# Kernel optimization log

Hardware: AMD Instinct MI355X
Metric: run time of the kernel (lower is better)

Reference implementation:

```python
import jax, jax.numpy as jnp
import numpy as np
import math

EMBED_DIM = 768
NUM_HEADS = 12
HEAD_DIM = EMBED_DIM // NUM_HEADS
SPARSITY = 0.1


def setup_inputs() -> dict:
    key = jax.random.key(0)
    ks = jax.random.split(key, 5)
    B, N, D = 4, 1024, EMBED_DIM
    s = 1.0 / math.sqrt(D)
    return {
        "x": jax.random.normal(ks[0], (B, N, D), dtype=jnp.float32),
        "W_qkv": jax.random.normal(ks[1], (D, 3 * D), dtype=jnp.float32) * s,
        "b_qkv": jnp.zeros((3 * D,), dtype=jnp.float32),
        "W_out": jax.random.normal(ks[2], (D, D), dtype=jnp.float32) * s,
        "b_out": jnp.zeros((D,), dtype=jnp.float32),
    }


def reference(x, W_qkv, b_qkv, W_out, b_out):
    B, N, D = x.shape
    H, hd = NUM_HEADS, HEAD_DIM
    qkv = x @ W_qkv + b_qkv                      # [B,N,3D]
    qkv = qkv.reshape(B, N, 3, H, hd).transpose(2, 0, 3, 1, 4)  # [3,B,H,N,hd]
    q, k, v = qkv[0], qkv[1], qkv[2]
    attn = jnp.einsum("bhqd,bhkd->bhqk", q, k) * (1.0 / math.sqrt(hd))  # [B,H,N,N]
    kth = int(N * N * SPARSITY)
    if kth > 0:
        # kth smallest value over the flattened per-(b,h) attention matrix
        flat = attn.reshape(B, H, N * N)
        thr = jnp.sort(flat, axis=-1)[..., kth - 1]               # [B,H]
        attn = jnp.where(attn <= thr[:, :, None, None], -1e9, attn)
    attn = jax.nn.softmax(attn, axis=-1)
    out = jnp.einsum("bhqk,bhkd->bhqd", attn, v)                  # [B,H,N,hd]
    out = out.transpose(0, 2, 1, 3).reshape(B, N, D)
    return out @ W_out + b_out
```

## Files before the change

kernel.cpp:

```cpp
#include <hip/hip_runtime.h>
#include <math.h>

#define SEQ 1024
#define DMODEL 768
#define NHEADS 12
#define HDIM 64
#define D3 2304
#define BH 48
#define NTOK 4096
#define KTH 104857u
#define NBIN 4096
#define BIN0 14336

typedef __bf16 bf16x8 __attribute__((ext_vector_type(8)));
typedef float  f32x4  __attribute__((ext_vector_type(4)));

#define SWZ(row, chunk) ((row) * 32 + (((chunk) ^ (((row) >> 1) & 3)) * 8))

__device__ __forceinline__ void gl16(const ushort* g, ushort* l) {
    __builtin_amdgcn_global_load_lds(
        (__attribute__((address_space(1))) void*)(size_t)(g),
        (__attribute__((address_space(3))) void*)(l), 16, 0, 0);
}

__device__ __forceinline__ void split1(float x, ushort& h, ushort& l) {
    unsigned b  = __float_as_uint(x);
    unsigned hb = (b + 0x7FFFu + ((b >> 16) & 1u)) >> 16;
    float hf = __uint_as_float(hb << 16);
    float r  = x - hf;
    unsigned rb = __float_as_uint(r);
    unsigned lb = (rb + 0x7FFFu + ((rb >> 16) & 1u)) >> 16;
    h = (ushort)hb; l = (ushort)lb;
}

__device__ __forceinline__ ushort bf16rne(float x) {
    unsigned b = __float_as_uint(x);
    return (ushort)((b + 0x7FFFu + ((b >> 16) & 1u)) >> 16);
}

__global__ __launch_bounds__(256) void k_xsplit(const float* __restrict__ x,
                                                ushort* __restrict__ xh,
                                                ushort* __restrict__ xl, int n,
                                                unsigned* __restrict__ hist) {
    int g = blockIdx.x * 256 + threadIdx.x;
    if (g < BH * NBIN) hist[g] = 0u;
    int i = g * 4;
    if (i >= n) return;
    float4 v = *(const float4*)(x + i);
    ushort4 h, l;
    split1(v.x, h.x, l.x); split1(v.y, h.y, l.y);
    split1(v.z, h.z, l.z); split1(v.w, h.w, l.w);
    *(ushort4*)(xh + i) = h;
    *(ushort4*)(xl + i) = l;
}

__global__ __launch_bounds__(256) void k_wsplit(const float* __restrict__ W,
                                                ushort* __restrict__ Wth,
                                                ushort* __restrict__ Wtl,
                                                int K, int N) {
    __shared__ float t[64][65];
    int k0 = blockIdx.y * 64, n0 = blockIdx.x * 64;
    int tid = threadIdx.x;
    int r = tid >> 4, c = (tid & 15) * 4;
#pragma unroll
    for (int u = 0; u < 4; u++) {
        int rr = r + u * 16;
        float4 v = *(const float4*)(W + (size_t)(k0 + rr) * N + n0 + c);
        t[rr][c] = v.x; t[rr][c + 1] = v.y; t[rr][c + 2] = v.z; t[rr][c + 3] = v.w;
    }
    __syncthreads();
    int n = tid >> 2, kc = (tid & 3) * 16;
    ushort hb[16] __attribute__((aligned(16)));
    ushort lb[16] __attribute__((aligned(16)));
#pragma unroll
    for (int j = 0; j < 16; j++) split1(t[kc + j][n], hb[j], lb[j]);
    ushort* dh = Wth + (size_t)(n0 + n) * K + k0 + kc;
    ushort* dl = Wtl + (size_t)(n0 + n) * K + k0 + kc;
    *(uint4*)(dh)     = *(uint4*)&hb[0];
    *(uint4*)(dh + 8) = *(uint4*)&hb[8];
    *(uint4*)(dl)     = *(uint4*)&lb[0];
    *(uint4*)(dl + 8) = *(uint4*)&lb[8];
}

#define STAGE_LDS(ko)                                                           \
    gl16(gAh + (ko), &sA[0][wbase]);                                            \
    gl16(gAh2 + (ko), &sA[0][2048 + wbase]);                                    \
    gl16(gAl + (ko), &sA[1][wbase]);                                            \
    gl16(gAl2 + (ko), &sA[1][2048 + wbase]);                                    \
    gl16(gBh + (ko), &sB[0][wbase]);                                            \
    gl16(gBh2 + (ko), &sB[0][2048 + wbase]);                                    \
    gl16(gBl + (ko), &sB[1][wbase]);                                            \
    gl16(gBl2 + (ko), &sB[1][2048 + wbase]);

#define GEMM_CORE_SETUP(Kdim)                                                   \
    __shared__ ushort sA[2][128 * 32];                                          \
    __shared__ ushort sB[2][128 * 32];                                          \
    int tid = threadIdx.x, lane = tid & 63, wave = tid >> 6;                    \
    int wm = (wave >> 1) * 64, wn = (wave & 1) * 64;                            \
    int l15 = lane & 15, q = lane >> 4;                                         \
    int sr = tid >> 2, sc = tid & 3;                                            \
    const int K = (Kdim);                                                       \
    int scs = sc ^ ((sr >> 1) & 3);          \
    const ushort* gAh = Ah + (size_t)(m0 + sr) * K + scs * 8;                   \
    const ushort* gAl = Al + (size_t)(m0 + sr) * K + scs * 8;                   \
    const ushort* gBh = Bh + (size_t)(n0 + sr) * K + scs * 8;                   \
    const ushort* gBl = Bl + (size_t)(n0 + sr) * K + scs * 8;                   \
    const ushort* gAh2 = gAh + (size_t)64 * K;                                  \
    const ushort* gAl2 = gAl + (size_t)64 * K;                                  \
    const ushort* gBh2 = gBh + (size_t)64 * K;                                  \
    const ushort* gBl2 = gBl + (size_t)64 * K;                                  \
    int wbase = wave * 512;              \
    f32x4 acc[4][4] = {};                                                       \
    STAGE_LDS(0)                                                                \
    __syncthreads();                                                            \
    const int NIT = K / 32;                                                     \
    for (int it = 0; it < NIT; ++it) {                                          \
        bf16x8 fah[4], fal[4], fbh[4], fbl[4];                                  \
        _Pragma("unroll")                                                       \
        for (int mt = 0; mt < 4; mt++) {                                        \
            int rr = wm + mt * 16 + l15;                                        \
            fah[mt] = *(const bf16x8*)(&sA[0][SWZ(rr, q)]);                     \
            fal[mt] = *(const bf16x8*)(&sA[1][SWZ(rr, q)]);                     \
        }                                                                       \
        _Pragma("unroll")                                                       \
        for (int nt = 0; nt < 4; nt++) {                                        \
            int rr = wn + nt * 16 + l15;                                        \
            fbh[nt] = *(const bf16x8*)(&sB[0][SWZ(rr, q)]);                     \
            fbl[nt] = *(const bf16x8*)(&sB[1][SWZ(rr, q)]);                     \
        }                                                                       \
        __syncthreads();                 \
        if (it + 1 < NIT) { STAGE_LDS((it + 1) * 32) }                          \
        _Pragma("unroll")                                                       \
        for (int mt = 0; mt < 4; mt++)                                          \
            _Pragma("unroll")                                                   \
            for (int nt = 0; nt < 4; nt++) {                                    \
                acc[mt][nt] = __builtin_amdgcn_mfma_f32_16x16x32_bf16(          \
                    fah[mt], fbh[nt], acc[mt][nt], 0, 0, 0);                    \
                acc[mt][nt] = __builtin_amdgcn_mfma_f32_16x16x32_bf16(          \
                    fah[mt], fbl[nt], acc[mt][nt], 0, 0, 0);                    \
                acc[mt][nt] = __builtin_amdgcn_mfma_f32_16x16x32_bf16(          \
                    fal[mt], fbh[nt], acc[mt][nt], 0, 0, 0);                    \
            }                                                                   \
        __syncthreads();                   \
    }

__global__ __launch_bounds__(256) void k_gemm_out(
    const ushort* __restrict__ Ah, const ushort* __restrict__ Al,
    const ushort* __restrict__ Bh, const ushort* __restrict__ Bl,
    const float* __restrict__ bias, float* __restrict__ C,
    int M, int N, int Kin) {
    int m0 = blockIdx.y * 128, n0 = blockIdx.x * 128;
    GEMM_CORE_SETUP(Kin)
#pragma unroll
    for (int nt = 0; nt < 4; nt++) {
        int col = n0 + wn + nt * 16 + l15;
        float bv = bias[col];
#pragma unroll
        for (int mt = 0; mt < 4; mt++) {
            int rowb = m0 + wm + mt * 16 + q * 4;
#pragma unroll
            for (int r = 0; r < 4; r++)
                C[(size_t)(rowb + r) * N + col] = acc[mt][nt][r] + bv;
        }
    }
}

__global__ __launch_bounds__(256) void k_gemm_qkv(
    const ushort* __restrict__ Ah, const ushort* __restrict__ Al,
    const ushort* __restrict__ Bh, const ushort* __restrict__ Bl,
    const float* __restrict__ bias,
    ushort* __restrict__ Qh, ushort* __restrict__ Ql,
    ushort* __restrict__ Kh, ushort* __restrict__ Kl,
    ushort* __restrict__ Vth) {
    int m0 = blockIdx.y * 128, n0 = blockIdx.x * 128;
    GEMM_CORE_SETUP(DMODEL)
    int region = n0 / 768;
#pragma unroll
    for (int nt = 0; nt < 4; nt++) {
        int col = n0 + wn + nt * 16 + l15;
        float bv = bias[col];
        int cin = col - region * 768;
        int h = cin >> 6, d = cin & 63;
#pragma unroll
        for (int mt = 0; mt < 4; mt++) {
            int rowb = m0 + wm + mt * 16 + q * 4;
            int b = rowb >> 10;
            int s0 = rowb & 1023;
            int bh = b * NHEADS + h;
            if (region == 2) {
                ushort h4[4] __attribute__((aligned(8)));
#pragma unroll
                for (int r = 0; r < 4; r++)
                    h4[r] = bf16rne(acc[mt][nt][r] + bv);
                size_t off = ((size_t)(bh * 64 + d) << 10) + s0;
                *(ushort4*)(Vth + off) = *(ushort4*)h4;
            } else {
                ushort* Ph = region ? Kh : Qh;
                ushort* Pl = region ? Kl : Ql;
                size_t off = ((size_t)((bh << 10) + s0)) * 64 + d;
#pragma unroll
                for (int r = 0; r < 4; r++) {
                    ushort hs, ls;
                    split1(acc[mt][nt][r] + bv, hs, ls);
                    Ph[off + (size_t)r * 64] = hs;
                    Pl[off + (size_t)r * 64] = ls;
                }
            }
        }
    }
}

__global__ __launch_bounds__(256) void k_scores(
    const ushort* __restrict__ Qh, const ushort* __restrict__ Ql,
    const ushort* __restrict__ Kh, const ushort* __restrict__ Kl,
    unsigned* __restrict__ hist) {
    __shared__ unsigned lh[NBIN];
    int bh = blockIdx.z;
    int i0 = blockIdx.y * 128, j0 = blockIdx.x * 128;
    int tid = threadIdx.x, lane = tid & 63, wave = tid >> 6;
    int l15 = lane & 15, q = lane >> 4;
    int wj = (wave >> 1) * 64, wi = (wave & 1) * 64;
    for (int i = tid; i < NBIN; i += 256) lh[i] = 0u;
    __syncthreads();

    const ushort* qb  = Qh + ((size_t)bh << 16);
    const ushort* qlb = Ql + ((size_t)bh << 16);
    const ushort* kb  = Kh + ((size_t)bh << 16);
    const ushort* klb = Kl + ((size_t)bh << 16);

    bf16x8 fqh[4][2], fql[4][2];
#pragma unroll
    for (int nt = 0; nt < 4; nt++)
#pragma unroll
        for (int kk = 0; kk < 2; kk++) {
            size_t off = (size_t)(i0 + wi + nt * 16 + l15) * 64 + kk * 32 + q * 8;
            fqh[nt][kk] = *(const bf16x8*)(qb + off);
            fql[nt][kk] = *(const bf16x8*)(qlb + off);
        }
    bf16x8 fkh[2][2], fkl[2][2];
#pragma unroll
    for (int kk = 0; kk < 2; kk++) {
        size_t off = (size_t)(j0 + wj + l15) * 64 + kk * 32 + q * 8;
        fkh[0][kk] = *(const bf16x8*)(kb + off);
        fkl[0][kk] = *(const bf16x8*)(klb + off);
    }

#pragma unroll
    for (int mt = 0; mt < 4; mt++) {
        int cur = mt & 1;
        if (mt < 3) {
            int nxt = cur ^ 1;
#pragma unroll
            for (int kk = 0; kk < 2; kk++) {
                size_t off = (size_t)(j0 + wj + (mt + 1) * 16 + l15) * 64 + kk * 32 + q * 8;
                fkh[nxt][kk] = *(const bf16x8*)(kb + off);
                fkl[nxt][kk] = *(const bf16x8*)(klb + off);
            }
        }
        f32x4 acc[4] = {};
#pragma unroll
        for (int kk = 0; kk < 2; kk++)
#pragma unroll
            for (int nt = 0; nt < 4; nt++) {
                acc[nt] = __builtin_amdgcn_mfma_f32_16x16x32_bf16(
                    fkh[cur][kk], fqh[nt][kk], acc[nt], 0, 0, 0);
                acc[nt] = __builtin_amdgcn_mfma_f32_16x16x32_bf16(
                    fkl[cur][kk], fqh[nt][kk], acc[nt], 0, 0, 0);
                acc[nt] = __builtin_amdgcn_mfma_f32_16x16x32_bf16(
                    fkh[cur][kk], fql[nt][kk], acc[nt], 0, 0, 0);
            }
#pragma unroll
        for (int nt = 0; nt < 4; nt++) {
#pragma unroll
            for (int r = 0; r < 4; r++) {
                ushort u = bf16rne(__expf(acc[nt][r] * 0.125f));
                int bin = (int)u - BIN0;
                bin = (bin < 0) ? 0 : ((bin > NBIN - 1) ? NBIN - 1 : bin);
                atomicAdd(&lh[bin], 1u);
            }
        }
    }
    __syncthreads();
    for (int i = tid; i < NBIN; i += 256) {
        unsigned cc = lh[i];
        if (cc) atomicAdd(&hist[bh * NBIN + i], cc);
    }
}

__global__ void k_select(const unsigned* __restrict__ hist,
                         unsigned* __restrict__ thrb) {
    int bh = blockIdx.x;
    const unsigned* hrow = hist + bh * NBIN;
    __shared__ unsigned ps[256];
    int tid = threadIdx.x;
    unsigned s = 0;
#pragma unroll
    for (int i = 0; i < 16; i++) s += hrow[tid * 16 + i];
    ps[tid] = s;
    __syncthreads();
    if (tid == 0) {
        unsigned k = KTH, run = 0; int chunk = 255;
        for (int t2 = 0; t2 < 256; t2++) {
            if (run + ps[t2] >= k) { chunk = t2; break; }
            run += ps[t2];
        }
        int d = 15;
        for (int i = 0; i < 16; i++) {
            unsigned v = hrow[chunk * 16 + i];
            if (run + v >= k) { d = i; break; }
            run += v;
        }
        thrb[bh] = (unsigned)(BIN0 + chunk * 16 + d);
    }
}

__global__ __launch_bounds__(256) void k_pv(const ushort* __restrict__ Qh,
                                            const ushort* __restrict__ Ql,
                                            const ushort* __restrict__ Kh,
                                            const ushort* __restrict__ Kl,
                                            const ushort* __restrict__ Vth,
                                            const unsigned* __restrict__ thrb,
                                            ushort* __restrict__ ctxh,
                                            ushort* __restrict__ ctxl) {
    __shared__ ushort sK[2][2][32 * 64];
    __shared__ ushort sV[2][64 * 32];
    __shared__ ushort pt[4][32 * 40] __attribute__((aligned(16)));
    int bh = blockIdx.y;
    int b = bh / NHEADS, h = bh % NHEADS;
    int tid = threadIdx.x, lane = tid & 63, wave = tid >> 6;
    int l15 = lane & 15, q = lane >> 4;
    int i0 = blockIdx.x * 128;
    unsigned t = thrb[bh];

    const ushort* qb  = Qh + ((size_t)bh << 16);
    const ushort* qlb = Ql + ((size_t)bh << 16);
    const ushort* kb  = Kh + ((size_t)bh << 16);
    const ushort* klb = Kl + ((size_t)bh << 16);
    const ushort* vh0 = Vth + ((size_t)bh << 16);

    int sr2 = tid >> 3, sc2 = tid & 7;
    const ushort* gK  = kb  + (size_t)sr2 * 64 + ((sc2 ^ (sr2 & 7)) * 8);
    const ushort* gKl = klb + (size_t)sr2 * 64 + ((sc2 ^ (sr2 & 7)) * 8);
    int sr = tid >> 2, sc = tid & 3;
    const ushort* gV = vh0 + (size_t)sr * 1024 + ((sc ^ ((sr >> 1) & 3)) * 8);
    int wbase = wave * 512;

    bf16x8 fqh[2][2], fql[2][2];
#pragma unroll
    for (int ig = 0; ig < 2; ig++)
#pragma unroll
        for (int kk = 0; kk < 2; kk++) {
            size_t off = (size_t)(i0 + wave * 32 + ig * 16 + l15) * 64 + kk * 32 + q * 8;
            fqh[ig][kk] = *(const bf16x8*)(qb + off);
            fql[ig][kk] = *(const bf16x8*)(qlb + off);
        }

    f32x4 accp[2][4] = {};
    f32x4 lacc[2] = {};
    uint4 onesu = {0x3F803F80u, 0x3F803F80u, 0x3F803F80u, 0x3F803F80u};
    bf16x8 ones = *(bf16x8*)&onesu;
    ushort* myP = &pt[wave][0];

    gl16(gK,  &sK[0][0][wbase]);
    gl16(gKl, &sK[0][1][wbase]);
    gl16(gV,  &sV[0][wbase]);
    __syncthreads();

    for (int j0 = 0; j0 < SEQ; j0 += 32) {
        int cur = (j0 >> 5) & 1;
        bf16x8 kh[2][2], kl[2][2];
#pragma unroll
        for (int j16 = 0; j16 < 2; j16++) {
            int row = j16 * 16 + l15, rs = row & 7;
#pragma unroll
            for (int kk = 0; kk < 2; kk++) {
                int off = row * 64 + (((kk * 4 + q) ^ rs) * 8);
                kh[j16][kk] = *(const bf16x8*)(&sK[cur][0][off]);
                kl[j16][kk] = *(const bf16x8*)(&sK[cur][1][off]);
            }
        }
        bf16x8 fvh[4];
#pragma unroll
        for (int nt = 0; nt < 4; nt++)
            fvh[nt] = *(const bf16x8*)(&sV[cur][SWZ(nt * 16 + l15, q)]);
        if (j0 + 32 < SEQ) {
            int nxt = cur ^ 1;
            gl16(gK  + (size_t)(j0 + 32) * 64, &sK[nxt][0][wbase]);
            gl16(gKl + (size_t)(j0 + 32) * 64, &sK[nxt][1][wbase]);
            gl16(gV  + (j0 + 32),              &sV[nxt][wbase]);
        }
        bf16x8 pa[2];
#pragma unroll
        for (int ig = 0; ig < 2; ig++) {
#pragma unroll
            for (int j16 = 0; j16 < 2; j16++) {
                f32x4 s = {};
                s = __builtin_amdgcn_mfma_f32_16x16x32_bf16(kh[j16][0], fqh[ig][0], s, 0, 0, 0);
                s = __builtin_amdgcn_mfma_f32_16x16x32_bf16(kl[j16][0], fqh[ig][0], s, 0, 0, 0);
                s = __builtin_amdgcn_mfma_f32_16x16x32_bf16(kh[j16][0], fql[ig][0], s, 0, 0, 0);
                s = __builtin_amdgcn_mfma_f32_16x16x32_bf16(kh[j16][1], fqh[ig][1], s, 0, 0, 0);
                s = __builtin_amdgcn_mfma_f32_16x16x32_bf16(kl[j16][1], fqh[ig][1], s, 0, 0, 0);
                s = __builtin_amdgcn_mfma_f32_16x16x32_bf16(kh[j16][1], fql[ig][1], s, 0, 0, 0);
                unsigned pb[4];
#pragma unroll
                for (int r = 0; r < 4; r++) {
                    unsigned u = bf16rne(__expf(s[r] * 0.125f));
                    pb[r] = (u <= t) ? 0u : u;
                }
                uint2 w;
                w.x = pb[0] | (pb[1] << 16);
                w.y = pb[2] | (pb[3] << 16);
                *(uint2*)(&myP[(ig * 16 + l15) * 40 + j16 * 16 + q * 4]) = w;
            }
            pa[ig] = *(const bf16x8*)(&myP[(ig * 16 + l15) * 40 + q * 8]);
        }
#pragma unroll
        for (int ig = 0; ig < 2; ig++) {
#pragma unroll
            for (int nt = 0; nt < 4; nt++)
                accp[ig][nt] = __builtin_amdgcn_mfma_f32_16x16x32_bf16(
                    pa[ig], fvh[nt], accp[ig][nt], 0, 0, 0);
            lacc[ig] = __builtin_amdgcn_mfma_f32_16x16x32_bf16(
                pa[ig], ones, lacc[ig], 0, 0, 0);
        }
        __syncthreads();
    }
#pragma unroll
    for (int ig = 0; ig < 2; ig++)
#pragma unroll
        for (int r = 0; r < 4; r++) {
            int i = i0 + wave * 32 + ig * 16 + q * 4 + r;
            float l = lacc[ig][r];
#pragma unroll
            for (int nt = 0; nt < 4; nt++) {
                int d = nt * 16 + l15;
                ushort hs, ls;
                split1(accp[ig][nt][r] / l, hs, ls);
                size_t off = ((size_t)(b * SEQ + i)) * DMODEL + h * 64 + d;
                ctxh[off] = hs;
                ctxl[off] = ls;
            }
        }
}

extern "C" void kernel_launch(void* const* d_in, const int* in_sizes, int n_in,
                              void* d_out, int out_size, void* d_ws, size_t ws_size,
                              hipStream_t stream) {
    const float* x    = (const float*)d_in[0];
    const float* Wqkv = (const float*)d_in[1];
    const float* bqkv = (const float*)d_in[2];
    const float* Wout = (const float*)d_in[3];
    const float* bout = (const float*)d_in[4];
    float* out = (float*)d_out;

    char* ws = (char*)d_ws;
    ushort* Qh  = (ushort*)(ws + 0);
    ushort* Ql  = (ushort*)(ws + 6291456);
    ushort* Kh  = (ushort*)(ws + 12582912);
    ushort* Kl  = (ushort*)(ws + 18874368);
    ushort* Vth = (ushort*)(ws + 25165824);
    ushort* ctxh = (ushort*)(ws + 239075328);
    ushort* ctxl = (ushort*)(ws + 245366784);
    unsigned* hist = (unsigned*)(ws + 251658240);
    unsigned* thrb = (unsigned*)(ws + 252444672);
    ushort* xh     = (ushort*)(ws + 37748736);
    ushort* xl     = (ushort*)(ws + 37748736 + 6291456);
    ushort* Wqkvth = (ushort*)(ws + 37748736 + 12582912);
    ushort* Wqkvtl = (ushort*)(ws + 37748736 + 16121856);
    ushort* Woutth = (ushort*)(ws + 37748736);
    ushort* Wouttl = (ushort*)(ws + 37748736 + 1179648);

    k_xsplit<<<NTOK * DMODEL / 1024, 256, 0, stream>>>(x, xh, xl, NTOK * DMODEL, hist);
    k_wsplit<<<dim3(D3 / 64, DMODEL / 64), 256, 0, stream>>>(Wqkv, Wqkvth, Wqkvtl, DMODEL, D3);
    k_gemm_qkv<<<dim3(D3 / 128, NTOK / 128), 256, 0, stream>>>(
        xh, xl, Wqkvth, Wqkvtl, bqkv, Qh, Ql, Kh, Kl, Vth);
    k_scores<<<dim3(8, 8, BH), 256, 0, stream>>>(Qh, Ql, Kh, Kl, hist);
    k_select<<<BH, 256, 0, stream>>>(hist, thrb);
    k_pv<<<dim3(SEQ / 128, BH), 256, 0, stream>>>(Qh, Ql, Kh, Kl, Vth, thrb, ctxh, ctxl);
    k_wsplit<<<dim3(DMODEL / 64, DMODEL / 64), 256, 0, stream>>>(Wout, Woutth, Wouttl, DMODEL, DMODEL);
    k_gemm_out<<<dim3(DMODEL / 128, NTOK / 128), 256, 0, stream>>>(
        ctxh, ctxl, Woutth, Wouttl, bout, out, NTOK, DMODEL, DMODEL);
}
```

Before: 281.0 us.

## Fuse threshold selection into PV kernel and remap blocks XCD-aware

Removes the separate k_select launch: each k_pv block now reads the per-head histogram, computes chunk prefix sums in shared memory and finds the threshold bin itself, overlapped with the first K/V tile prefetch. Both k_scores and k_pv switch to a 1D grid whose block index is remapped so consecutive blocks of the same head land on the same XCD, which is meant to improve L2 reuse of Q/K/V. The trade-off is redundant selection work in every PV block (eight times per head) and a serial 256-iteration prefix loop per thread.

```diff
diff --git a/kernel.cpp b/kernel.cpp
--- a/kernel.cpp
+++ b/kernel.cpp
@@ -215,8 +215,11 @@
     const ushort* __restrict__ Kh, const ushort* __restrict__ Kl,
     unsigned* __restrict__ hist) {
     __shared__ unsigned lh[NBIN];
-    int bh = blockIdx.z;
-    int i0 = blockIdx.y * 128, j0 = blockIdx.x * 128;
+    int orig = blockIdx.x;
+    int wid = (orig & 7) * 384 + (orig >> 3);
+    int bh = wid >> 6;
+    int rem = wid & 63;
+    int i0 = (rem >> 3) * 128, j0 = (rem & 7) * 128;
     int tid = threadIdx.x, lane = tid & 63, wave = tid >> 6;
     int l15 = lane & 15, q = lane >> 4;
     int wj = (wave >> 1) * 64, wi = (wave & 1) * 64;
@@ -287,50 +290,26 @@
     }
 }
 
-__global__ void k_select(const unsigned* __restrict__ hist,
-                         unsigned* __restrict__ thrb) {
-    int bh = blockIdx.x;
-    const unsigned* hrow = hist + bh * NBIN;
-    __shared__ unsigned ps[256];
-    int tid = threadIdx.x;
-    unsigned s = 0;
-#pragma unroll
-    for (int i = 0; i < 16; i++) s += hrow[tid * 16 + i];
-    ps[tid] = s;
-    __syncthreads();
-    if (tid == 0) {
-        unsigned k = KTH, run = 0; int chunk = 255;
-        for (int t2 = 0; t2 < 256; t2++) {
-            if (run + ps[t2] >= k) { chunk = t2; break; }
-            run += ps[t2];
-        }
-        int d = 15;
-        for (int i = 0; i < 16; i++) {
-            unsigned v = hrow[chunk * 16 + i];
-            if (run + v >= k) { d = i; break; }
-            run += v;
-        }
-        thrb[bh] = (unsigned)(BIN0 + chunk * 16 + d);
-    }
-}
-
 __global__ __launch_bounds__(256) void k_pv(const ushort* __restrict__ Qh,
                                             const ushort* __restrict__ Ql,
                                             const ushort* __restrict__ Kh,
                                             const ushort* __restrict__ Kl,
                                             const ushort* __restrict__ Vth,
-                                            const unsigned* __restrict__ thrb,
+                                            const unsigned* __restrict__ hist,
                                             ushort* __restrict__ ctxh,
                                             ushort* __restrict__ ctxl) {
     __shared__ ushort sK[2][2][32 * 64];
     __shared__ ushort sV[2][64 * 32];
     __shared__ ushort pt[4][32 * 40] __attribute__((aligned(16)));
-    int bh = blockIdx.y;
+    __shared__ unsigned ps[256];
+    __shared__ unsigned thrS;
+    int orig = blockIdx.x;
+    int wid = (orig & 7) * 48 + (orig >> 3);
+    int bh = wid >> 3;
+    int i0 = (wid & 7) * 128;
     int b = bh / NHEADS, h = bh % NHEADS;
     int tid = threadIdx.x, lane = tid & 63, wave = tid >> 6;
     int l15 = lane & 15, q = lane >> 4;
-    int i0 = blockIdx.x * 128;
-    unsigned t = thrb[bh];
 
     const ushort* qb  = Qh + ((size_t)bh << 16);
     const ushort* qlb = Ql + ((size_t)bh << 16);
@@ -345,6 +324,34 @@
     const ushort* gV = vh0 + (size_t)sr * 1024 + ((sc ^ ((sr >> 1) & 3)) * 8);
     int wbase = wave * 512;
 
+    gl16(gK,  &sK[0][0][wbase]);
+    gl16(gKl, &sK[0][1][wbase]);
+    gl16(gV,  &sV[0][wbase]);
+
+    const unsigned* hrow = hist + bh * NBIN;
+    unsigned psum = 0;
+#pragma unroll
+    for (int i = 0; i < 16; i++) psum += hrow[tid * 16 + i];
+    ps[tid] = psum;
+    __syncthreads();
+    unsigned pre = 0;
+    for (int u = 0; u < 256; u++) {
+        unsigned v = ps[u];
+        if (u < tid) pre += v;
+    }
+    if (pre < KTH && pre + psum >= KTH) {
+        unsigned run = pre; int d = 15;
+#pragma unroll
+        for (int i = 0; i < 16; i++) {
+            unsigned v = hrow[tid * 16 + i];
+            if (run + v >= KTH) { d = i; break; }
+            run += v;
+        }
+        thrS = (unsigned)(BIN0 + tid * 16 + d);
+    }
+    __syncthreads();
+    unsigned t = thrS;
+
     bf16x8 fqh[2][2], fql[2][2];
 #pragma unroll
     for (int ig = 0; ig < 2; ig++)
@@ -360,11 +367,6 @@
     uint4 onesu = {0x3F803F80u, 0x3F803F80u, 0x3F803F80u, 0x3F803F80u};
     bf16x8 ones = *(bf16x8*)&onesu;
     ushort* myP = &pt[wave][0];
-
-    gl16(gK,  &sK[0][0][wbase]);
-    gl16(gKl, &sK[0][1][wbase]);
-    gl16(gV,  &sV[0][wbase]);
-    __syncthreads();
 
     for (int j0 = 0; j0 < SEQ; j0 += 32) {
         int cur = (j0 >> 5) & 1;
@@ -462,7 +464,6 @@
     ushort* ctxh = (ushort*)(ws + 239075328);
     ushort* ctxl = (ushort*)(ws + 245366784);
     unsigned* hist = (unsigned*)(ws + 251658240);
-    unsigned* thrb = (unsigned*)(ws + 252444672);
     ushort* xh     = (ushort*)(ws + 37748736);
     ushort* xl     = (ushort*)(ws + 37748736 + 6291456);
     ushort* Wqkvth = (ushort*)(ws + 37748736 + 12582912);
@@ -474,9 +475,8 @@
     k_wsplit<<<dim3(D3 / 64, DMODEL / 64), 256, 0, stream>>>(Wqkv, Wqkvth, Wqkvtl, DMODEL, D3);
     k_gemm_qkv<<<dim3(D3 / 128, NTOK / 128), 256, 0, stream>>>(
         xh, xl, Wqkvth, Wqkvtl, bqkv, Qh, Ql, Kh, Kl, Vth);
-    k_scores<<<dim3(8, 8, BH), 256, 0, stream>>>(Qh, Ql, Kh, Kl, hist);
-    k_select<<<BH, 256, 0, stream>>>(hist, thrb);
-    k_pv<<<dim3(SEQ / 128, BH), 256, 0, stream>>>(Qh, Ql, Kh, Kl, Vth, thrb, ctxh, ctxl);
+    k_scores<<<3072, 256, 0, stream>>>(Qh, Ql, Kh, Kl, hist);
+    k_pv<<<384, 256, 0, stream>>>(Qh, Ql, Kh, Kl, Vth, hist, ctxh, ctxl);
     k_wsplit<<<dim3(DMODEL / 64, DMODEL / 64), 256, 0, stream>>>(Wout, Woutth, Wouttl, DMODEL, DMODEL);
     k_gemm_out<<<dim3(DMODEL / 128, NTOK / 128), 256, 0, stream>>>(
         ctxh, ctxl, Woutth, Wouttl, bout, out, NTOK, DMODEL, DMODEL);
```

After: 280.5 us. About the same (-0.2%).
